# Performance work log

Hardware: AMD Instinct MI355X
Metric: run time of the kernel (lower is better)

## Reference

```python
import jax, jax.numpy as jnp
import numpy as np

NUM_HEADS = 12


def setup_inputs() -> dict:
    key = jax.random.key(0)
    k1, k2, k3 = jax.random.split(key, 3)
    B, N, D = 16, 1024, 768
    x = jax.random.normal(k1, (B, N, D), dtype=jnp.float32)
    qkv_w = jax.random.normal(k2, (D, 3 * D), dtype=jnp.float32) * (1.0 / np.sqrt(D))
    proj_w = jax.random.normal(k3, (D, D), dtype=jnp.float32) * (1.0 / np.sqrt(D))
    proj_b = jnp.zeros((D,), dtype=jnp.float32)
    return {"x": x, "qkv_w": qkv_w, "proj_w": proj_w, "proj_b": proj_b}


def reference(x, qkv_w, proj_w, proj_b):
    B, N, D = x.shape
    H = NUM_HEADS
    hd = D // H
    scale = hd ** -0.5
    qkv = jnp.einsum('bnd,de->bne', x, qkv_w)
    qkv = qkv.reshape(B, N, 3, H, hd).transpose(2, 0, 3, 1, 4)
    q, k, v = qkv[0], qkv[1], qkv[2]
    # attention scores [B, H, N, N]
    attn = jnp.einsum('bhqd,bhkd->bhqk', q, k) * scale
    attn = jax.nn.softmax(attn, axis=-1)
    out = jnp.einsum('bhqk,bhkd->bhqd', attn, v)
    out = out.transpose(0, 2, 1, 3).reshape(B, N, D)
    # output projection
    return jnp.einsum('bnd,de->bne', out, proj_w) + proj_b
```

## Files before the change

kernel.cpp:

```cpp
#include <hip/hip_runtime.h>
#include <cstdint>
#include <cstddef>

typedef float f32x4 __attribute__((ext_vector_type(4)));
typedef __bf16 bf16x8 __attribute__((ext_vector_type(8)));

#define BB 16
#define SEQ 1024
#define DMODEL 768
#define NHEAD 12
#define HDIM 64
#define MTOT (BB * SEQ)
#define NQKV (3 * DMODEL)
#define NQK (2 * DMODEL)
#define QSCALE 0.18033688011112042f

static __device__ __forceinline__ unsigned short f2bf(float f) {
  unsigned int u = __builtin_bit_cast(unsigned int, f);
  u += 0x7fffu + ((u >> 16) & 1u);
  return (unsigned short)(u >> 16);
}

static __device__ __forceinline__ unsigned cvt_pk_bf16(float lo, float hi) {
  unsigned r;
  asm("v_cvt_pk_bf16_f32 %0, %1, %2" : "=v"(r) : "v"(lo), "v"(hi));
  return r;
}

static __device__ __forceinline__ void gload_lds16(const void* g, void* l) {
  __builtin_amdgcn_global_load_lds((__attribute__((address_space(1))) void*)g,
                                   (__attribute__((address_space(3))) void*)l,
                                   16, 0, 0);
}

__global__ void k_cvt_bf16(const float4* __restrict__ in, ushort4* __restrict__ out, int n4) {
  int stride = gridDim.x * blockDim.x;
  for (int i = blockIdx.x * blockDim.x + threadIdx.x; i < n4; i += stride) {
    float4 v = in[i];
    ushort4 o;
    o.x = f2bf(v.x); o.y = f2bf(v.y); o.z = f2bf(v.z); o.w = f2bf(v.w);
    out[i] = o;
  }
}

__global__ void k_transpose_bf16(const float* __restrict__ in, unsigned short* __restrict__ out,
                                 int R, int C, int scaleN) {
  __shared__ float tile[32][33];
  int tx = threadIdx.x & 31, ty = threadIdx.x >> 5;
  int c0 = blockIdx.x * 32, r0 = blockIdx.y * 32;
#pragma unroll
  for (int i = 0; i < 4; ++i)
    tile[ty + i * 8][tx] = in[(size_t)(r0 + ty + i * 8) * C + c0 + tx];
  __syncthreads();
#pragma unroll
  for (int i = 0; i < 4; ++i) {
    const int n = c0 + ty + i * 8;
    float v = tile[tx][ty + i * 8];
    if (n < scaleN) v *= QSCALE;
    out[(size_t)n * R + r0 + tx] = f2bf(v);
  }
}

template <int MODE>
__global__ __launch_bounds__(256, 3) void k_gemm_bt(
    const unsigned short* __restrict__ A, const unsigned short* __restrict__ Bt,
    int M, int N, int K,
    float* __restrict__ outF, const float* __restrict__ bias,
    unsigned short* __restrict__ QK, unsigned short* __restrict__ Vt) {
  __shared__ __align__(16) unsigned short As[128 * 64];
  __shared__ __align__(16) unsigned short Bs[128 * 64];
  const int tid = threadIdx.x;
  const int lane = tid & 63, wid = tid >> 6;
  const int ln15 = lane & 15, lh = lane >> 4;
  const int wr = wid >> 1, wc = wid & 1;
  const int m0 = blockIdx.x * 128, n0 = blockIdx.y * 128;
  f32x4 acc[4][4] = {};
  const int srow = lane >> 3;
  const int sblk = ((lane & 7) ^ srow) * 8;
  const int swz = (ln15 & 7) << 3;
  const int nk = K >> 6;

  for (int kt = 0; kt < nk; ++kt) {
    const int k0 = kt * 64;
#pragma unroll
    for (int c = 0; c < 4; ++c) {
      const int ch = wid * 4 + c;
      const int row = ch * 8 + srow;
      gload_lds16(A + (size_t)(m0 + row) * K + k0 + sblk, &As[ch * 512]);
      gload_lds16(Bt + (size_t)(n0 + row) * K + k0 + sblk, &Bs[ch * 512]);
    }
    __syncthreads();
#pragma unroll
    for (int kk = 0; kk < 2; ++kk) {
      const int kc = kk * 32 + lh * 8;
      bf16x8 af[4], bfv[4];
#pragma unroll
      for (int mt = 0; mt < 4; ++mt)
        af[mt] = *reinterpret_cast<const bf16x8*>(
            &As[(wr * 64 + mt * 16 + ln15) * 64 + (kc ^ swz)]);
#pragma unroll
      for (int nn = 0; nn < 4; ++nn)
        bfv[nn] = *reinterpret_cast<const bf16x8*>(
            &Bs[(wc * 64 + nn * 16 + ln15) * 64 + (kc ^ swz)]);
#pragma unroll
      for (int mt = 0; mt < 4; ++mt)
#pragma unroll
        for (int nn = 0; nn < 4; ++nn)
          acc[mt][nn] = __builtin_amdgcn_mfma_f32_16x16x32_bf16(af[mt], bfv[nn], acc[mt][nn], 0, 0, 0);
    }
    __syncthreads();
  }

#pragma unroll
  for (int mt = 0; mt < 4; ++mt) {
#pragma unroll
    for (int nn = 0; nn < 4; ++nn) {
      const int nb = n0 + wc * 64 + nn * 16;
      const int mb = m0 + wr * 64 + mt * 16 + lh * 4;
      if (MODE == 0) {
#pragma unroll
        for (int r = 0; r < 4; ++r)
          outF[(size_t)(mb + r) * N + nb + ln15] = acc[mt][nn][r] + bias[nb + ln15];
      } else if (nb < NQK) {
#pragma unroll
        for (int r = 0; r < 4; ++r)
          QK[(size_t)(mb + r) * NQK + nb + ln15] = f2bf(acc[mt][nn][r]);
      } else {
        const int rr = nb + ln15 - NQK;
        const int h = rr >> 6, d = rr & 63;
        const int b = mb >> 10, nr0 = mb & 1023;
        ushort4 u;
        u.x = f2bf(acc[mt][nn][0]); u.y = f2bf(acc[mt][nn][1]);
        u.z = f2bf(acc[mt][nn][2]); u.w = f2bf(acc[mt][nn][3]);
        *reinterpret_cast<ushort4*>(
            &Vt[(((size_t)b * NHEAD + h) * HDIM + d) * SEQ + nr0]) = u;
      }
    }
  }
}

__global__ __launch_bounds__(512) void k_attn(
    const unsigned short* __restrict__ QKn, const unsigned short* __restrict__ Vt,
    unsigned short* __restrict__ O) {
  __shared__ __align__(16) unsigned short Ks[2][64 * 64];
  __shared__ __align__(16) unsigned short Vs[2][64 * 64];
  __shared__ __align__(16) unsigned short Ps[8][16 * 72];
  const int tid = threadIdx.x;
  const int lane = tid & 63, w = tid >> 6;
  const int ln15 = lane & 15, lh = lane >> 4;
  const int o = blockIdx.x;
  const int sid = (o & 7) * 192 + (o >> 3);
  const int qb = sid & 7;
  const int bhid = sid >> 3;
  const int h = bhid % NHEAD;
  const int b = bhid / NHEAD;
  const size_t bh = (size_t)(b * NHEAD + h);
  const unsigned short* Qbase = QKn + (size_t)(b * SEQ + qb * 128 + w * 16) * NQK + h * HDIM;
  const unsigned short* Kbase = QKn + (size_t)(b * SEQ) * NQK + DMODEL + h * HDIM;
  const unsigned short* Vbase = Vt + bh * HDIM * SEQ;

  const int srow = lane >> 3;
  const int sblk = ((lane & 7) ^ srow) * 8;
  const int swz = (ln15 & 7) << 3;

  auto stage = [&](int kb, int s) {
    const int row = w * 8 + srow;
    gload_lds16(Kbase + (size_t)(kb * 64 + row) * NQK + sblk, &Ks[s][w * 512]);
    gload_lds16(Vbase + (size_t)row * SEQ + kb * 64 + sblk, &Vs[s][w * 512]);
  };

  bf16x8 aq[2];
#pragma unroll
  for (int ch = 0; ch < 2; ++ch)
    aq[ch] = *reinterpret_cast<const bf16x8*>(Qbase + (size_t)ln15 * NQK + ch * 32 + lh * 8);

  f32x4 acc[4] = {};
  float mr = -1e30f, lr = 0.f;

  stage(0, 0);
  for (int kb = 0; kb < SEQ / 64; ++kb) {
    const int s = kb & 1;
    __syncthreads();
    if (kb + 1 < SEQ / 64) stage(kb + 1, s ^ 1);

    f32x4 sv[4] = {};
    __builtin_amdgcn_s_setprio(1);
#pragma unroll
    for (int t = 0; t < 4; ++t) {
#pragma unroll
      for (int ch = 0; ch < 2; ++ch) {
        bf16x8 bk = *reinterpret_cast<const bf16x8*>(
            &Ks[s][(t * 16 + ln15) * 64 + ((ch * 32 + lh * 8) ^ swz)]);
        sv[t] = __builtin_amdgcn_mfma_f32_16x16x32_bf16(bk, aq[ch], sv[t], 0, 0, 0);
      }
    }
    __builtin_amdgcn_s_setprio(0);

    float bm;
    {
      const float a0 = fmaxf(fmaxf(sv[0][0], sv[0][1]), fmaxf(sv[0][2], sv[0][3]));
      const float a1 = fmaxf(fmaxf(sv[1][0], sv[1][1]), fmaxf(sv[1][2], sv[1][3]));
      const float a2 = fmaxf(fmaxf(sv[2][0], sv[2][1]), fmaxf(sv[2][2], sv[2][3]));
      const float a3 = fmaxf(fmaxf(sv[3][0], sv[3][1]), fmaxf(sv[3][2], sv[3][3]));
      bm = fmaxf(fmaxf(a0, a1), fmaxf(a2, a3));
    }
    bm = fmaxf(bm, __shfl_xor(bm, 16));
    bm = fmaxf(bm, __shfl_xor(bm, 32));
    const int grow = __any(bm > mr + 8.f);
    float al = 1.f;
    if (grow) {
      const float mn = fmaxf(mr, bm);
      al = __builtin_amdgcn_exp2f(mr - mn);
      mr = mn;
    }
#pragma unroll
    for (int t = 0; t < 4; ++t)
#pragma unroll
      for (int r = 0; r < 4; ++r) sv[t][r] = __builtin_amdgcn_exp2f(sv[t][r] - mr);
    float rs;
    {
      const float a0 = (sv[0][0] + sv[0][1]) + (sv[0][2] + sv[0][3]);
      const float a1 = (sv[1][0] + sv[1][1]) + (sv[1][2] + sv[1][3]);
      const float a2 = (sv[2][0] + sv[2][1]) + (sv[2][2] + sv[2][3]);
      const float a3 = (sv[3][0] + sv[3][1]) + (sv[3][2] + sv[3][3]);
      rs = (a0 + a1) + (a2 + a3);
    }
    rs += __shfl_xor(rs, 16);
    rs += __shfl_xor(rs, 32);
    lr = lr * al + rs;
    if (grow) {
      float alq[4];
#pragma unroll
      for (int r = 0; r < 4; ++r) alq[r] = __shfl(al, lh * 4 + r);
#pragma unroll
      for (int dt = 0; dt < 4; ++dt)
#pragma unroll
        for (int r = 0; r < 4; ++r) acc[dt][r] *= alq[r];
    }

#pragma unroll
    for (int t = 0; t < 4; ++t) {
      uint2 u;
      u.x = cvt_pk_bf16(sv[t][0], sv[t][1]);
      u.y = cvt_pk_bf16(sv[t][2], sv[t][3]);
      *reinterpret_cast<uint2*>(&Ps[w][ln15 * 72 + t * 16 + lh * 4]) = u;
    }

    bf16x8 ap[2];
#pragma unroll
    for (int ch = 0; ch < 2; ++ch)
      ap[ch] = *reinterpret_cast<const bf16x8*>(&Ps[w][ln15 * 72 + ch * 32 + lh * 8]);
    __builtin_amdgcn_s_setprio(1);
#pragma unroll
    for (int dt = 0; dt < 4; ++dt) {
#pragma unroll
      for (int ch = 0; ch < 2; ++ch) {
        bf16x8 bv = *reinterpret_cast<const bf16x8*>(
            &Vs[s][(dt * 16 + ln15) * 64 + ((ch * 32 + lh * 8) ^ swz)]);
        acc[dt] = __builtin_amdgcn_mfma_f32_16x16x32_bf16(ap[ch], bv, acc[dt], 0, 0, 0);
      }
    }
    __builtin_amdgcn_s_setprio(0);
  }

  float lrq[4];
#pragma unroll
  for (int r = 0; r < 4; ++r) lrq[r] = 1.0f / __shfl(lr, lh * 4 + r);
  const int qrow = qb * 128 + w * 16 + lh * 4;
#pragma unroll
  for (int dt = 0; dt < 4; ++dt)
#pragma unroll
    for (int r = 0; r < 4; ++r)
      O[((size_t)b * SEQ + qrow + r) * DMODEL + h * 64 + dt * 16 + ln15] = f2bf(acc[dt][r] * lrq[r]);
}

extern "C" void kernel_launch(void* const* d_in, const int* in_sizes, int n_in,
                              void* d_out, int out_size, void* d_ws, size_t ws_size,
                              hipStream_t stream) {
  const float* x      = (const float*)d_in[0];
  const float* qkv_w  = (const float*)d_in[1];
  const float* proj_w = (const float*)d_in[2];
  const float* proj_b = (const float*)d_in[3];
  float* out = (float*)d_out;

  char* ws = (char*)d_ws;
  const size_t SZ_XB   = (size_t)MTOT * DMODEL * 2;
  const size_t SZ_WQT  = (size_t)NQKV * DMODEL * 2;
  const size_t SZ_WPT  = (size_t)DMODEL * DMODEL * 2;
  const size_t SZ_QK   = (size_t)MTOT * NQK * 2;
  const size_t SZ_VT   = (size_t)BB * NHEAD * HDIM * SEQ * 2;
  unsigned short* Xb   = (unsigned short*)ws;
  unsigned short* WqT  = (unsigned short*)(ws + SZ_XB);
  unsigned short* WpT  = (unsigned short*)(ws + SZ_XB + SZ_WQT);
  unsigned short* QKn  = (unsigned short*)(ws + SZ_XB + SZ_WQT + SZ_WPT);
  unsigned short* Vt   = (unsigned short*)(ws + SZ_XB + SZ_WQT + SZ_WPT + SZ_QK);
  if (ws_size < SZ_XB + SZ_WQT + SZ_WPT + SZ_QK + SZ_VT) return;

  k_cvt_bf16<<<2048, 256, 0, stream>>>((const float4*)x, (ushort4*)Xb, MTOT * DMODEL / 4);
  k_transpose_bf16<<<dim3(NQKV / 32, DMODEL / 32), 256, 0, stream>>>(qkv_w, WqT, DMODEL, NQKV, DMODEL);
  k_transpose_bf16<<<dim3(DMODEL / 32, DMODEL / 32), 256, 0, stream>>>(proj_w, WpT, DMODEL, DMODEL, 0);
  k_gemm_bt<1><<<dim3(MTOT / 128, NQKV / 128), 256, 0, stream>>>(
      Xb, WqT, MTOT, NQKV, DMODEL, nullptr, nullptr, QKn, Vt);
  k_attn<<<BB * NHEAD * 8, 512, 0, stream>>>(QKn, Vt, Xb);
  k_gemm_bt<0><<<dim3(MTOT / 128, DMODEL / 128), 256, 0, stream>>>(
      Xb, WpT, MTOT, DMODEL, DMODEL, out, proj_b, nullptr, nullptr);
}
```

Measured before the change: 186.1 us.

## Fold running max into MFMA init and compute row sums via MFMA with ones

The attention inner loop now seeds the score accumulators with the negated running max, so the per-element subtraction before exp2 goes away. The rescale check uses a per-lane threshold test before any cross-lane reduction, so the max shuffles only run when a rescale is needed. Row sums are computed with an extra MFMA against a ones vector instead of VALU adds and shuffles. The cost is two extra MFMAs per block, and the denominator now accumulates bf16-rounded probabilities.

```diff
diff --git a/kernel.cpp b/kernel.cpp
--- a/kernel.cpp
+++ b/kernel.cpp
@@ -174,8 +174,14 @@
   for (int ch = 0; ch < 2; ++ch)
     aq[ch] = *reinterpret_cast<const bf16x8*>(Qbase + (size_t)ln15 * NQK + ch * 32 + lh * 8);
 
+  bf16x8 onesb;
+#pragma unroll
+  for (int i = 0; i < 8; ++i) onesb[i] = (__bf16)1.0f;
+
   f32x4 acc[4] = {};
-  float mr = -1e30f, lr = 0.f;
+  f32x4 accl = {};
+  float mr = 0.f;
+  f32x4 cinit = {};
 
   stage(0, 0);
   for (int kb = 0; kb < SEQ / 64; ++kb) {
@@ -183,7 +189,9 @@
     __syncthreads();
     if (kb + 1 < SEQ / 64) stage(kb + 1, s ^ 1);
 
-    f32x4 sv[4] = {};
+    f32x4 sv[4];
+#pragma unroll
+    for (int t = 0; t < 4; ++t) sv[t] = cinit;
     __builtin_amdgcn_s_setprio(1);
 #pragma unroll
     for (int t = 0; t < 4; ++t) {
@@ -196,47 +204,41 @@
     }
     __builtin_amdgcn_s_setprio(0);
 
-    float bm;
+    float pm;
     {
       const float a0 = fmaxf(fmaxf(sv[0][0], sv[0][1]), fmaxf(sv[0][2], sv[0][3]));
       const float a1 = fmaxf(fmaxf(sv[1][0], sv[1][1]), fmaxf(sv[1][2], sv[1][3]));
       const float a2 = fmaxf(fmaxf(sv[2][0], sv[2][1]), fmaxf(sv[2][2], sv[2][3]));
       const float a3 = fmaxf(fmaxf(sv[3][0], sv[3][1]), fmaxf(sv[3][2], sv[3][3]));
-      bm = fmaxf(fmaxf(a0, a1), fmaxf(a2, a3));
-    }
-    bm = fmaxf(bm, __shfl_xor(bm, 16));
-    bm = fmaxf(bm, __shfl_xor(bm, 32));
-    const int grow = __any(bm > mr + 8.f);
-    float al = 1.f;
-    if (grow) {
-      const float mn = fmaxf(mr, bm);
-      al = __builtin_amdgcn_exp2f(mr - mn);
-      mr = mn;
-    }
+      pm = fmaxf(fmaxf(a0, a1), fmaxf(a2, a3));
+    }
+    if (__any(pm > 8.f)) {
+      float bmf = pm;
+      bmf = fmaxf(bmf, __shfl_xor(bmf, 16));
+      bmf = fmaxf(bmf, __shfl_xor(bmf, 32));
+      const float delta = fmaxf(bmf, 0.f);
+      const float al = __builtin_amdgcn_exp2f(-delta);
+#pragma unroll
+      for (int t = 0; t < 4; ++t)
+#pragma unroll
+        for (int r = 0; r < 4; ++r) sv[t][r] -= delta;
+      mr += delta;
+      cinit[0] = -mr; cinit[1] = -mr; cinit[2] = -mr; cinit[3] = -mr;
+      float alq[4];
+#pragma unroll
+      for (int r = 0; r < 4; ++r) alq[r] = __shfl(al, lh * 4 + r);
+#pragma unroll
+      for (int dt = 0; dt < 4; ++dt)
+#pragma unroll
+        for (int r = 0; r < 4; ++r) acc[dt][r] *= alq[r];
+#pragma unroll
+      for (int r = 0; r < 4; ++r) accl[r] *= alq[r];
+    }
+
 #pragma unroll
     for (int t = 0; t < 4; ++t)
 #pragma unroll
-      for (int r = 0; r < 4; ++r) sv[t][r] = __builtin_amdgcn_exp2f(sv[t][r] - mr);
-    float rs;
-    {
-      const float a0 = (sv[0][0] + sv[0][1]) + (sv[0][2] + sv[0][3]);
-      const float a1 = (sv[1][0] + sv[1][1]) + (sv[1][2] + sv[1][3]);
-      const float a2 = (sv[2][0] + sv[2][1]) + (sv[2][2] + sv[2][3]);
-      const float a3 = (sv[3][0] + sv[3][1]) + (sv[3][2] + sv[3][3]);
-      rs = (a0 + a1) + (a2 + a3);
-    }
-    rs += __shfl_xor(rs, 16);
-    rs += __shfl_xor(rs, 32);
-    lr = lr * al + rs;
-    if (grow) {
-      float alq[4];
-#pragma unroll
-      for (int r = 0; r < 4; ++r) alq[r] = __shfl(al, lh * 4 + r);
-#pragma unroll
-      for (int dt = 0; dt < 4; ++dt)
-#pragma unroll
-        for (int r = 0; r < 4; ++r) acc[dt][r] *= alq[r];
-    }
+      for (int r = 0; r < 4; ++r) sv[t][r] = __builtin_amdgcn_exp2f(sv[t][r]);
 
 #pragma unroll
     for (int t = 0; t < 4; ++t) {
@@ -252,6 +254,9 @@
       ap[ch] = *reinterpret_cast<const bf16x8*>(&Ps[w][ln15 * 72 + ch * 32 + lh * 8]);
     __builtin_amdgcn_s_setprio(1);
 #pragma unroll
+    for (int ch = 0; ch < 2; ++ch)
+      accl = __builtin_amdgcn_mfma_f32_16x16x32_bf16(ap[ch], onesb, accl, 0, 0, 0);
+#pragma unroll
     for (int dt = 0; dt < 4; ++dt) {
 #pragma unroll
       for (int ch = 0; ch < 2; ++ch) {
@@ -263,15 +268,13 @@
     __builtin_amdgcn_s_setprio(0);
   }
 
-  float lrq[4];
-#pragma unroll
-  for (int r = 0; r < 4; ++r) lrq[r] = 1.0f / __shfl(lr, lh * 4 + r);
   const int qrow = qb * 128 + w * 16 + lh * 4;
 #pragma unroll
   for (int dt = 0; dt < 4; ++dt)
 #pragma unroll
     for (int r = 0; r < 4; ++r)
-      O[((size_t)b * SEQ + qrow + r) * DMODEL + h * 64 + dt * 16 + ln15] = f2bf(acc[dt][r] * lrq[r]);
+      O[((size_t)b * SEQ + qrow + r) * DMODEL + h * 64 + dt * 16 + ln15] =
+          f2bf(acc[dt][r] / accl[r]);
 }
 
 extern "C" void kernel_launch(void* const* d_in, const int* in_sizes, int n_in,
```

Result: faster. 174.0 us (-6.5%).
